# Optimization experiments

Hardware: AMD Instinct MI355X
Metric: run time of the kernel (lower is better)

Reference implementation:

```python
import jax, jax.numpy as jnp
import numpy as np

N_NODES = 50000
N_EDGES = 400000
NFEAT, NHID, NOUT, NCLASS = 512, 256, 256, 8


def _glorot(key, shape):
    lim = float(np.sqrt(6.0 / (shape[0] + shape[1])))
    return jax.random.uniform(key, shape, jnp.float32, -lim, lim)


def setup_inputs() -> dict:
    key = jax.random.key(0)
    ks = jax.random.split(key, 8)
    x = jax.random.normal(ks[0], (N_NODES, NFEAT), jnp.float32)
    edge_index = jax.random.randint(ks[1], (2, N_EDGES), 0, N_NODES, jnp.int32)
    # learnable edge weight logits (init 1 - eps in the module; trained => generic values)
    edge_w_params = jnp.ones((N_EDGES,), jnp.float32) * 0.9999
    W1 = _glorot(ks[2], (NFEAT, NHID)); b1 = jnp.zeros((NHID,), jnp.float32)
    W2 = _glorot(ks[3], (NHID, NHID)); b2 = jnp.zeros((NHID,), jnp.float32)
    W3 = _glorot(ks[4], (NHID, NOUT)); b3 = jnp.zeros((NOUT,), jnp.float32)
    Wlin = _glorot(ks[5], (NHID + NHID + NOUT, NCLASS))
    blin = jnp.zeros((NCLASS,), jnp.float32)
    return {"x": x, "edge_index": edge_index, "edge_w_params": edge_w_params,
            "W1": W1, "b1": b1, "W2": W2, "b2": b2, "W3": W3, "b3": b3,
            "Wlin": Wlin, "blin": blin}


def _gcn_conv(x, W, b, src, dst, ew, n):
    """PyG GCNConv with add_self_loops=True.
    Self-loop weight is 1 (fill_value). norm = d^-1/2[src] * w * d^-1/2[dst].
    Self-loop contribution handled analytically (no edge concat).
    """
    deg = jax.ops.segment_sum(ew, dst, num_segments=n) + 1.0  # +1 self-loop weight
    dinv = jnp.where(deg > 0, jax.lax.rsqrt(deg), 0.0)
    norm = dinv[src] * ew * dinv[dst]                          # [E]
    h = x @ W                                                  # [n, out]
    agg = jax.ops.segment_sum(h[src] * norm[:, None], dst, num_segments=n)
    agg = agg + h * (dinv * dinv)[:, None]                     # self loops
    return agg + b


def reference(x, edge_index, edge_w_params, W1, b1, W2, b2, W3, b3, Wlin, blin):
    n = x.shape[0]
    src, dst = edge_index[0], edge_index[1]
    ew = jax.nn.sigmoid(edge_w_params)
    ones_ew = jnp.ones_like(ew)
    x1 = jax.nn.relu(_gcn_conv(x, W1, b1, src, dst, ew, n))    # dropout: eval mode (identity)
    x2 = jax.nn.relu(_gcn_conv(x1, W2, b2, src, dst, ew, n))
    x3 = _gcn_conv(x2, W3, b3, src, dst, ones_ew, n)           # gc3 called without edge_weight
    logits = jnp.concatenate((x1, x2, x3), axis=1) @ Wlin + blin
    return jax.nn.log_softmax(logits, axis=1)
```

## Files before the change

### kernel.cpp

```cpp
#include <hip/hip_runtime.h>
#include <math.h>

#define N_NODES 50000
#define N_EDGES 400000
#define M_PAD 50048
#define NFEAT 512
#define NHID 256
#define NCLASS 8
#define SCAN_BLOCKS ((N_NODES + 255) / 256)

typedef unsigned short u16;
typedef __attribute__((ext_vector_type(8))) unsigned short u16x8;
typedef __attribute__((ext_vector_type(8))) short s16x8;
typedef __attribute__((ext_vector_type(4))) float f32x4;

__device__ __forceinline__ float bf2f(u16 u) {
    union { unsigned int i; float f; } v; v.i = ((unsigned int)u) << 16; return v.f;
}
__device__ __forceinline__ float bf2f_hi(unsigned int packed) {
    union { unsigned int i; float f; } v; v.i = packed & 0xffff0000u; return v.f;
}
__device__ __forceinline__ float bf2f_lo(unsigned int packed) {
    union { unsigned int i; float f; } v; v.i = packed << 16; return v.f;
}
__device__ __forceinline__ u16 f2bf(float f) {
    union { float f; unsigned int i; } v; v.f = f;
    unsigned int r = v.i + 0x7fffu + ((v.i >> 16) & 1u);
    return (u16)(r >> 16);
}


__global__ void init_k(float* deg, int* cnt, int* cur) {
    int i = blockIdx.x * blockDim.x + threadIdx.x;
    if (i < N_NODES) { deg[i] = 1.0f; cnt[i] = 0; cur[i] = 0; }
}

__global__ void edge_deg_k(const float* __restrict__ p, const int* __restrict__ dst,
                           float* __restrict__ deg, int* __restrict__ cnt,
                           float* __restrict__ ew_out) {
    int e = blockIdx.x * blockDim.x + threadIdx.x;
    if (e >= N_EDGES) return;
    float ew = 1.0f / (1.0f + expf(-p[e]));
    ew_out[e] = ew;
    int d = dst[e];
    atomicAdd(&deg[d], ew);
    atomicAdd(&cnt[d], 1);
}

__global__ void finalize_dinv_k(float* __restrict__ deg, const int* __restrict__ cnt,
                                float* __restrict__ dinv3) {
    int i = blockIdx.x * blockDim.x + threadIdx.x;
    if (i < N_NODES) {
        deg[i]   = 1.0f / sqrtf(deg[i]);
        dinv3[i] = 1.0f / sqrtf(1.0f + (float)cnt[i]);
    }
}

__global__ __launch_bounds__(256) void scan1_k(const int* __restrict__ cnt,
                                               int* __restrict__ row_start,
                                               int* __restrict__ bsum) {
    __shared__ int tmp[256];
    int t = threadIdx.x;
    int g = blockIdx.x * 256 + t;
    int v = (g < N_NODES) ? cnt[g] : 0;
    tmp[t] = v;
    __syncthreads();
    #pragma unroll
    for (int off = 1; off < 256; off <<= 1) {
        int u = (t >= off) ? tmp[t - off] : 0;
        __syncthreads();
        tmp[t] += u;
        __syncthreads();
    }
    if (g < N_NODES) row_start[g] = tmp[t] - v;
    if (t == 255) bsum[blockIdx.x] = tmp[255];
}

__global__ __launch_bounds__(256) void scan2_k(int* __restrict__ bsum) {
    __shared__ int tmp[256];
    int t = threadIdx.x;
    int v = (t < SCAN_BLOCKS) ? bsum[t] : 0;
    tmp[t] = v;
    __syncthreads();
    #pragma unroll
    for (int off = 1; off < 256; off <<= 1) {
        int u = (t >= off) ? tmp[t - off] : 0;
        __syncthreads();
        tmp[t] += u;
        __syncthreads();
    }
    if (t < SCAN_BLOCKS) bsum[t] = tmp[t] - v;
}

__global__ __launch_bounds__(256) void scan3_k(int* __restrict__ row_start,
                                               const int* __restrict__ bsum) {
    int t = threadIdx.x;
    int g = blockIdx.x * 256 + t;
    if (g < N_NODES) row_start[g] += bsum[blockIdx.x];
    if (g == 0) row_start[N_NODES] = N_EDGES;
}

__global__ void fill_k(const int* __restrict__ src, const int* __restrict__ dst,
                       const float* __restrict__ ew, const float* __restrict__ dinv,
                       const float* __restrict__ dinv3,
                       const int* __restrict__ row_start, int* __restrict__ cur,
                       uint2* __restrict__ ep, uint2* __restrict__ ep3) {
    int e = blockIdx.x * blockDim.x + threadIdx.x;
    if (e >= N_EDGES) return;
    int s = src[e], d = dst[e];
    float w  = dinv[s] * ew[e] * dinv[d];
    float w3 = dinv3[s] * dinv3[d];
    int p = atomicAdd(&cur[d], 1);
    int slot = row_start[d] + p;
    ep[slot]  = make_uint2((unsigned int)s, __float_as_uint(w));
    ep3[slot] = make_uint2((unsigned int)s, __float_as_uint(w3));
}


__global__ void wtrans_all_k(const float* __restrict__ W1, const float* __restrict__ W2,
                             const float* __restrict__ W3, u16* __restrict__ wt1,
                             u16* __restrict__ wt2, u16* __restrict__ wt3) {
    int idx = blockIdx.x * 256 + threadIdx.x;
    const float* W; u16* Wt; int K;
    if (idx < 256 * 512)           { W = W1; Wt = wt1; K = 512; }
    else if (idx < 256 * 512 + 256 * 256) { idx -= 256 * 512; W = W2; Wt = wt2; K = 256; }
    else if (idx < 256 * 512 + 2 * 256 * 256) { idx -= 256 * 512 + 256 * 256; W = W3; Wt = wt3; K = 256; }
    else return;
    int n = idx / K, k = idx - n * K;
    Wt[(size_t)n * K + k] = f2bf(W[(size_t)k * 256 + n]);
}

__global__ void zeropad_k(u16* a, u16* b) {
    int i = blockIdx.x * 256 + threadIdx.x;
    if (i < (M_PAD - N_NODES) * 256) {
        a[(size_t)N_NODES * 256 + i] = 0;
        b[(size_t)N_NODES * 256 + i] = 0;
    }
}


__device__ __forceinline__ u16x8 ldcvt_f32(const float* p, bool ok) {
    u16x8 o = {0, 0, 0, 0, 0, 0, 0, 0};
    if (ok) {
        float4 a = *(const float4*)p;
        float4 b = *(const float4*)(p + 4);
        o[0] = f2bf(a.x); o[1] = f2bf(a.y); o[2] = f2bf(a.z); o[3] = f2bf(a.w);
        o[4] = f2bf(b.x); o[5] = f2bf(b.y); o[6] = f2bf(b.z); o[7] = f2bf(b.w);
    }
    return o;
}

template <bool AF32>
__global__ __launch_bounds__(256) void gemm_bf16_k(const void* __restrict__ Ap,
                                                   const u16* __restrict__ BT,
                                                   u16* __restrict__ C, int K) {
    __shared__ u16 Asl[128 * 40];
    __shared__ u16 Bsl[128 * 40];
    int tid = threadIdx.x;
    int lane = tid & 63;
    int wid = tid >> 6;
    int wm = wid >> 1, wn = wid & 1;
    int row0 = blockIdx.x * 128;
    int col0 = blockIdx.y * 128;

    int c0 = tid, c1 = tid + 256;
    int ar0 = c0 >> 2, ak0 = (c0 & 3) << 3;
    int ar1 = c1 >> 2, ak1 = (c1 & 3) << 3;
    const u16*   A16 = (const u16*)Ap;
    const float* A32 = (const float*)Ap;
    bool ok0 = (row0 + ar0) < N_NODES;
    bool ok1 = (row0 + ar1) < N_NODES;
    const u16* Ag0 = A16 + (size_t)(row0 + ar0) * K + ak0;
    const u16* Ag1 = A16 + (size_t)(row0 + ar1) * K + ak1;
    const float* Af0 = A32 + (size_t)(row0 + ar0) * K + ak0;
    const float* Af1 = A32 + (size_t)(row0 + ar1) * K + ak1;
    const u16* Bg0 = BT + (size_t)(col0 + ar0) * K + ak0;
    const u16* Bg1 = BT + (size_t)(col0 + ar1) * K + ak1;
    int la0 = ar0 * 40 + ak0, la1 = ar1 * 40 + ak1;

    u16x8 ra0, ra1;
    if (AF32) { ra0 = ldcvt_f32(Af0, ok0); ra1 = ldcvt_f32(Af1, ok1); }
    else      { ra0 = *(const u16x8*)Ag0;  ra1 = *(const u16x8*)Ag1; }
    u16x8 rb0 = *(const u16x8*)Bg0;
    u16x8 rb1 = *(const u16x8*)Bg1;

    f32x4 acc[4][4] = {};

    int arow = wm * 64 + (lane & 15);
    int bcol = wn * 64 + (lane & 15);
    int kg = (lane >> 4) << 3;

    int nt = K >> 5;
    for (int t = 0; t < nt; ++t) {
        __syncthreads();
        *(u16x8*)&Asl[la0] = ra0; *(u16x8*)&Asl[la1] = ra1;
        *(u16x8*)&Bsl[la0] = rb0; *(u16x8*)&Bsl[la1] = rb1;
        __syncthreads();
        if (t + 1 < nt) {
            int ko = (t + 1) << 5;
            if (AF32) { ra0 = ldcvt_f32(Af0 + ko, ok0); ra1 = ldcvt_f32(Af1 + ko, ok1); }
            else      { ra0 = *(const u16x8*)(Ag0 + ko); ra1 = *(const u16x8*)(Ag1 + ko); }
            rb0 = *(const u16x8*)(Bg0 + ko);
            rb1 = *(const u16x8*)(Bg1 + ko);
        }
        s16x8 af[4], bf[4];
        #pragma unroll
        for (int m = 0; m < 4; ++m)
            af[m] = *(const s16x8*)&Asl[(arow + m * 16) * 40 + kg];
        #pragma unroll
        for (int n = 0; n < 4; ++n)
            bf[n] = *(const s16x8*)&Bsl[(bcol + n * 16) * 40 + kg];
        #pragma unroll
        for (int m = 0; m < 4; ++m)
            #pragma unroll
            for (int n = 0; n < 4; ++n)
                acc[m][n] = __builtin_amdgcn_mfma_f32_16x16x32_bf16(af[m], bf[n], acc[m][n], 0, 0, 0);
    }

    int crow0 = row0 + wm * 64 + ((lane >> 4) << 2);
    int ccol  = col0 + wn * 64 + (lane & 15);
    #pragma unroll
    for (int m = 0; m < 4; ++m)
        #pragma unroll
        for (int n = 0; n < 4; ++n)
            #pragma unroll
            for (int r = 0; r < 4; ++r)
                C[(size_t)(crow0 + m * 16 + r) * 256 + ccol + n * 16] = f2bf(acc[m][n][r]);
}


template <bool RELU>
__global__ __launch_bounds__(256) void gather_k(const u16* __restrict__ h,
                                                const int* __restrict__ row_start,
                                                const uint2* __restrict__ ep,
                                                const float* __restrict__ dinv,
                                                const float* __restrict__ bias,
                                                u16* __restrict__ outb) {
    int node = blockIdx.x * 4 + (threadIdx.x >> 6);
    if (node >= N_NODES) return;
    int lane = threadIdx.x & 63;

    float di = dinv[node];
    float sw = di * di;
    uint2 hv = *(const uint2*)(h + (size_t)node * 256 + lane * 4);
    float4 acc;
    acc.x = bf2f_lo(hv.x) * sw; acc.y = bf2f_hi(hv.x) * sw;
    acc.z = bf2f_lo(hv.y) * sw; acc.w = bf2f_hi(hv.y) * sw;

    int beg = row_start[node], end = row_start[node + 1];
    int j = beg;
    for (; j + 4 <= end; j += 4) {
        uint2 e0 = ep[j], e1 = ep[j + 1], e2 = ep[j + 2], e3 = ep[j + 3];
        uint2 u0 = *(const uint2*)(h + (size_t)e0.x * 256 + lane * 4);
        uint2 u1 = *(const uint2*)(h + (size_t)e1.x * 256 + lane * 4);
        uint2 u2 = *(const uint2*)(h + (size_t)e2.x * 256 + lane * 4);
        uint2 u3 = *(const uint2*)(h + (size_t)e3.x * 256 + lane * 4);
        float w0 = __uint_as_float(e0.y), w1 = __uint_as_float(e1.y);
        float w2 = __uint_as_float(e2.y), w3 = __uint_as_float(e3.y);
        acc.x += bf2f_lo(u0.x) * w0; acc.y += bf2f_hi(u0.x) * w0;
        acc.z += bf2f_lo(u0.y) * w0; acc.w += bf2f_hi(u0.y) * w0;
        acc.x += bf2f_lo(u1.x) * w1; acc.y += bf2f_hi(u1.x) * w1;
        acc.z += bf2f_lo(u1.y) * w1; acc.w += bf2f_hi(u1.y) * w1;
        acc.x += bf2f_lo(u2.x) * w2; acc.y += bf2f_hi(u2.x) * w2;
        acc.z += bf2f_lo(u2.y) * w2; acc.w += bf2f_hi(u2.y) * w2;
        acc.x += bf2f_lo(u3.x) * w3; acc.y += bf2f_hi(u3.x) * w3;
        acc.z += bf2f_lo(u3.y) * w3; acc.w += bf2f_hi(u3.y) * w3;
    }
    for (; j < end; ++j) {
        uint2 e = ep[j];
        float w = __uint_as_float(e.y);
        uint2 uv = *(const uint2*)(h + (size_t)e.x * 256 + lane * 4);
        acc.x += bf2f_lo(uv.x) * w; acc.y += bf2f_hi(uv.x) * w;
        acc.z += bf2f_lo(uv.y) * w; acc.w += bf2f_hi(uv.y) * w;
    }
    float4 bv = ((const float4*)bias)[lane];
    acc.x += bv.x; acc.y += bv.y; acc.z += bv.z; acc.w += bv.w;
    if (RELU) {
        acc.x = fmaxf(acc.x, 0.f); acc.y = fmaxf(acc.y, 0.f);
        acc.z = fmaxf(acc.z, 0.f); acc.w = fmaxf(acc.w, 0.f);
    }
    uint2 o;
    o.x = (unsigned int)f2bf(acc.x) | ((unsigned int)f2bf(acc.y) << 16);
    o.y = (unsigned int)f2bf(acc.z) | ((unsigned int)f2bf(acc.w) << 16);
    *(uint2*)(outb + (size_t)node * 256 + lane * 4) = o;
}


template <bool FIRST>
__global__ __launch_bounds__(256) void logits_acc_k(const u16* __restrict__ x,
                                                    const float* __restrict__ Wlin,
                                                    const float* __restrict__ blin,
                                                    float* __restrict__ logits, int seg) {
    __shared__ float Ws[256 * 8];
    int tid = threadIdx.x;
    const float* Wseg = Wlin + (size_t)seg * 256 * 8;
    for (int i = tid; i < 2048; i += 256) Ws[i] = Wseg[i];
    __syncthreads();
    int row = blockIdx.x * 32 + (tid >> 3);
    int c = tid & 7;
    if (row >= N_NODES) return;
    const u16* xr = x + (size_t)row * 256;
    float acc = 0.f;
    for (int k8 = 0; k8 < 32; ++k8) {
        u16x8 v = *(const u16x8*)&xr[k8 * 8];
        #pragma unroll
        for (int i = 0; i < 8; ++i) acc += bf2f(v[i]) * Ws[(k8 * 8 + i) * 8 + c];
    }
    float* lp = &logits[(size_t)row * 8 + c];
    if (FIRST) *lp = acc + blin[c];
    else       *lp += acc;
}

__global__ void log_softmax_k(const float* __restrict__ logits, float* __restrict__ out) {
    int row = blockIdx.x * blockDim.x + threadIdx.x;
    if (row >= N_NODES) return;
    float4 a = *(const float4*)&logits[(size_t)row * 8];
    float4 b = *(const float4*)&logits[(size_t)row * 8 + 4];
    float m = fmaxf(fmaxf(fmaxf(a.x, a.y), fmaxf(a.z, a.w)),
                    fmaxf(fmaxf(b.x, b.y), fmaxf(b.z, b.w)));
    float s = expf(a.x - m) + expf(a.y - m) + expf(a.z - m) + expf(a.w - m)
            + expf(b.x - m) + expf(b.y - m) + expf(b.z - m) + expf(b.w - m);
    float ls = logf(s) + m;
    float* o = &out[(size_t)row * 8];
    o[0] = a.x - ls; o[1] = a.y - ls; o[2] = a.z - ls; o[3] = a.w - ls;
    o[4] = b.x - ls; o[5] = b.y - ls; o[6] = b.z - ls; o[7] = b.w - ls;
}


extern "C" void kernel_launch(void* const* d_in, const int* in_sizes, int n_in,
                              void* d_out, int out_size, void* d_ws, size_t ws_size,
                              hipStream_t stream) {
    const float* x    = (const float*)d_in[0];
    const int*   ei   = (const int*)d_in[1];
    const float* ewp  = (const float*)d_in[2];
    const float* W1   = (const float*)d_in[3];
    const float* b1   = (const float*)d_in[4];
    const float* W2   = (const float*)d_in[5];
    const float* b2   = (const float*)d_in[6];
    const float* W3   = (const float*)d_in[7];
    const float* b3   = (const float*)d_in[8];
    const float* Wlin = (const float*)d_in[9];
    const float* blin = (const float*)d_in[10];
    float* out = (float*)d_out;

    const int* src = ei;
    const int* dst = ei + N_EDGES;

    float* ws = (float*)d_ws;
    float* ew     = ws;
    float* dinv   = ew + N_EDGES;
    float* dinv3  = dinv + N_NODES;
    float* logits = dinv3 + N_NODES;
    int* cnt       = (int*)(logits + (size_t)N_NODES * 8);
    int* cur       = cnt + N_NODES;
    int* row_start = cur + N_NODES;
    int* bsum      = row_start + N_NODES + 1;
    uint2* ep  = (uint2*)(((uintptr_t)(bsum + SCAN_BLOCKS) + 127) & ~(uintptr_t)127);
    uint2* ep3 = ep + N_EDGES;
    u16* hb  = (u16*)(ep3 + N_EDGES);
    u16* x1b = hb  + (size_t)M_PAD * 256;
    u16* x2b = x1b + (size_t)M_PAD * 256;
    u16* x3b = x2b + (size_t)M_PAD * 256;
    u16* wt1 = x3b + (size_t)M_PAD * 256;
    u16* wt2 = wt1 + 256 * 512;
    u16* wt3 = wt2 + 256 * 256;

    dim3 blk(256);
    int nodeBlocks  = (N_NODES + 255) / 256;
    int edgeBlocks  = (N_EDGES + 255) / 256;
    int gathBlocks  = (N_NODES + 3) / 4;
    int rowBlocks32 = (N_NODES + 31) / 32;
    dim3 gemmGrid(M_PAD / 128, 2);

    init_k<<<nodeBlocks, blk, 0, stream>>>(dinv, cnt, cur);
    edge_deg_k<<<edgeBlocks, blk, 0, stream>>>(ewp, dst, dinv, cnt, ew);
    finalize_dinv_k<<<nodeBlocks, blk, 0, stream>>>(dinv, cnt, dinv3);
    scan1_k<<<SCAN_BLOCKS, blk, 0, stream>>>(cnt, row_start, bsum);
    scan2_k<<<1, blk, 0, stream>>>(bsum);
    scan3_k<<<SCAN_BLOCKS, blk, 0, stream>>>(row_start, bsum);
    fill_k<<<edgeBlocks, blk, 0, stream>>>(src, dst, ew, dinv, dinv3, row_start, cur, ep, ep3);

    wtrans_all_k<<<(256 * 512 + 2 * 256 * 256 + 255) / 256, blk, 0, stream>>>(
        W1, W2, W3, wt1, wt2, wt3);
    zeropad_k<<<48, blk, 0, stream>>>(x1b, x2b);

    gemm_bf16_k<true><<<gemmGrid, blk, 0, stream>>>(x, wt1, hb, NFEAT);
    gather_k<true><<<gathBlocks, blk, 0, stream>>>(hb, row_start, ep, dinv, b1, x1b);
    logits_acc_k<true><<<rowBlocks32, blk, 0, stream>>>(x1b, Wlin, blin, logits, 0);

    gemm_bf16_k<false><<<gemmGrid, blk, 0, stream>>>(x1b, wt2, hb, NHID);
    gather_k<true><<<gathBlocks, blk, 0, stream>>>(hb, row_start, ep, dinv, b2, x2b);
    logits_acc_k<false><<<rowBlocks32, blk, 0, stream>>>(x2b, Wlin, blin, logits, 1);

    gemm_bf16_k<false><<<gemmGrid, blk, 0, stream>>>(x2b, wt3, hb, NHID);
    gather_k<false><<<gathBlocks, blk, 0, stream>>>(hb, row_start, ep3, dinv3, b3, x3b);
    logits_acc_k<false><<<rowBlocks32, blk, 0, stream>>>(x3b, Wlin, blin, logits, 2);

    log_softmax_k<<<nodeBlocks, blk, 0, stream>>>(logits, out);
}
```

Baseline: 319.1 us.

## Fold scan fixup into consumers, merge setup kernels, fuse softmax, unroll gather

Drops the scan3 pass. Fill and gather now add the per-block offset bsum[node>>8] to row_start as they read it, and scan2 writes the final row_start sentinel. The weight-transpose and zero-pad kernels are merged into one launch, and log-softmax is folded into the last logits kernel using shuffles across the 8 class lanes. The gather loop is unrolled to 8 edges to keep more loads in flight. Together these remove three launches and some global traffic, at the cost of an extra bsum lookup on every CSR access and higher register pressure in gather.

```diff
diff --git a/kernel.cpp b/kernel.cpp
--- a/kernel.cpp
+++ b/kernel.cpp
@@ -76,7 +76,8 @@
     if (t == 255) bsum[blockIdx.x] = tmp[255];
 }
 
-__global__ __launch_bounds__(256) void scan2_k(int* __restrict__ bsum) {
+__global__ __launch_bounds__(256) void scan2_k(int* __restrict__ bsum,
+                                               int* __restrict__ row_start) {
     __shared__ int tmp[256];
     int t = threadIdx.x;
     int v = (t < SCAN_BLOCKS) ? bsum[t] : 0;
@@ -90,20 +91,14 @@
         __syncthreads();
     }
     if (t < SCAN_BLOCKS) bsum[t] = tmp[t] - v;
-}
-
-__global__ __launch_bounds__(256) void scan3_k(int* __restrict__ row_start,
-                                               const int* __restrict__ bsum) {
-    int t = threadIdx.x;
-    int g = blockIdx.x * 256 + t;
-    if (g < N_NODES) row_start[g] += bsum[blockIdx.x];
-    if (g == 0) row_start[N_NODES] = N_EDGES;
+    if (t == SCAN_BLOCKS - 1) row_start[N_NODES] = v;
 }
 
 __global__ void fill_k(const int* __restrict__ src, const int* __restrict__ dst,
                        const float* __restrict__ ew, const float* __restrict__ dinv,
                        const float* __restrict__ dinv3,
-                       const int* __restrict__ row_start, int* __restrict__ cur,
+                       const int* __restrict__ row_start, const int* __restrict__ bsum,
+                       int* __restrict__ cur,
                        uint2* __restrict__ ep, uint2* __restrict__ ep3) {
     int e = blockIdx.x * blockDim.x + threadIdx.x;
     if (e >= N_EDGES) return;
@@ -111,30 +106,33 @@
     float w  = dinv[s] * ew[e] * dinv[d];
     float w3 = dinv3[s] * dinv3[d];
     int p = atomicAdd(&cur[d], 1);
-    int slot = row_start[d] + p;
+    int slot = row_start[d] + bsum[d >> 8] + p;
     ep[slot]  = make_uint2((unsigned int)s, __float_as_uint(w));
     ep3[slot] = make_uint2((unsigned int)s, __float_as_uint(w3));
 }
 
 
-__global__ void wtrans_all_k(const float* __restrict__ W1, const float* __restrict__ W2,
-                             const float* __restrict__ W3, u16* __restrict__ wt1,
-                             u16* __restrict__ wt2, u16* __restrict__ wt3) {
+#define WT_TOTAL (256 * 512 + 2 * 256 * 256)
+#define ZP_TOTAL ((M_PAD - N_NODES) * 256)
+
+__global__ void wtrans_zp_k(const float* __restrict__ W1, const float* __restrict__ W2,
+                            const float* __restrict__ W3, u16* __restrict__ wt1,
+                            u16* __restrict__ wt2, u16* __restrict__ wt3,
+                            u16* __restrict__ zp_a, u16* __restrict__ zp_b) {
     int idx = blockIdx.x * 256 + threadIdx.x;
-    const float* W; u16* Wt; int K;
-    if (idx < 256 * 512)           { W = W1; Wt = wt1; K = 512; }
-    else if (idx < 256 * 512 + 256 * 256) { idx -= 256 * 512; W = W2; Wt = wt2; K = 256; }
-    else if (idx < 256 * 512 + 2 * 256 * 256) { idx -= 256 * 512 + 256 * 256; W = W3; Wt = wt3; K = 256; }
-    else return;
-    int n = idx / K, k = idx - n * K;
-    Wt[(size_t)n * K + k] = f2bf(W[(size_t)k * 256 + n]);
-}
-
-__global__ void zeropad_k(u16* a, u16* b) {
-    int i = blockIdx.x * 256 + threadIdx.x;
-    if (i < (M_PAD - N_NODES) * 256) {
-        a[(size_t)N_NODES * 256 + i] = 0;
-        b[(size_t)N_NODES * 256 + i] = 0;
+    if (idx < WT_TOTAL) {
+        const float* W; u16* Wt; int K;
+        if (idx < 256 * 512)                  { W = W1; Wt = wt1; K = 512; }
+        else if (idx < 256 * 512 + 256 * 256) { idx -= 256 * 512; W = W2; Wt = wt2; K = 256; }
+        else                                  { idx -= 256 * 512 + 256 * 256; W = W3; Wt = wt3; K = 256; }
+        int n = idx / K, k = idx - n * K;
+        Wt[(size_t)n * K + k] = f2bf(W[(size_t)k * 256 + n]);
+        return;
+    }
+    int z = idx - WT_TOTAL;
+    if (z < ZP_TOTAL) {
+        zp_a[(size_t)N_NODES * 256 + z] = 0;
+        zp_b[(size_t)N_NODES * 256 + z] = 0;
     }
 }
 
@@ -178,14 +176,13 @@
     const u16* Bg1 = BT + (size_t)(col0 + ar1) * K + ak1;
     int la0 = ar0 * 40 + ak0, la1 = ar1 * 40 + ak1;
 
-    u16x8 ra0, ra1;
+    u16x8 ra0, ra1, rb0, rb1;
     if (AF32) { ra0 = ldcvt_f32(Af0, ok0); ra1 = ldcvt_f32(Af1, ok1); }
     else      { ra0 = *(const u16x8*)Ag0;  ra1 = *(const u16x8*)Ag1; }
-    u16x8 rb0 = *(const u16x8*)Bg0;
-    u16x8 rb1 = *(const u16x8*)Bg1;
+    rb0 = *(const u16x8*)Bg0;
+    rb1 = *(const u16x8*)Bg1;
 
     f32x4 acc[4][4] = {};
-
     int arow = wm * 64 + (lane & 15);
     int bcol = wn * 64 + (lane & 15);
     int kg = (lane >> 4) << 3;
@@ -229,9 +226,15 @@
 }
 
 
+__device__ __forceinline__ void fma4(float4& acc, uint2 u, float w) {
+    acc.x += bf2f_lo(u.x) * w; acc.y += bf2f_hi(u.x) * w;
+    acc.z += bf2f_lo(u.y) * w; acc.w += bf2f_hi(u.y) * w;
+}
+
 template <bool RELU>
 __global__ __launch_bounds__(256) void gather_k(const u16* __restrict__ h,
                                                 const int* __restrict__ row_start,
+                                                const int* __restrict__ bsum,
                                                 const uint2* __restrict__ ep,
                                                 const float* __restrict__ dinv,
                                                 const float* __restrict__ bias,
@@ -247,31 +250,38 @@
     acc.x = bf2f_lo(hv.x) * sw; acc.y = bf2f_hi(hv.x) * sw;
     acc.z = bf2f_lo(hv.y) * sw; acc.w = bf2f_hi(hv.y) * sw;
 
-    int beg = row_start[node], end = row_start[node + 1];
+    int beg = row_start[node] + bsum[node >> 8];
+    int end = row_start[node + 1] + bsum[(node + 1) >> 8];
     int j = beg;
+    for (; j + 8 <= end; j += 8) {
+        uint2 e0 = ep[j],     e1 = ep[j + 1], e2 = ep[j + 2], e3 = ep[j + 3];
+        uint2 e4 = ep[j + 4], e5 = ep[j + 5], e6 = ep[j + 6], e7 = ep[j + 7];
+        uint2 u0 = *(const uint2*)(h + (size_t)e0.x * 256 + lane * 4);
+        uint2 u1 = *(const uint2*)(h + (size_t)e1.x * 256 + lane * 4);
+        uint2 u2 = *(const uint2*)(h + (size_t)e2.x * 256 + lane * 4);
+        uint2 u3 = *(const uint2*)(h + (size_t)e3.x * 256 + lane * 4);
+        uint2 u4 = *(const uint2*)(h + (size_t)e4.x * 256 + lane * 4);
+        uint2 u5 = *(const uint2*)(h + (size_t)e5.x * 256 + lane * 4);
+        uint2 u6 = *(const uint2*)(h + (size_t)e6.x * 256 + lane * 4);
+        uint2 u7 = *(const uint2*)(h + (size_t)e7.x * 256 + lane * 4);
+        fma4(acc, u0, __uint_as_float(e0.y)); fma4(acc, u1, __uint_as_float(e1.y));
+        fma4(acc, u2, __uint_as_float(e2.y)); fma4(acc, u3, __uint_as_float(e3.y));
+        fma4(acc, u4, __uint_as_float(e4.y)); fma4(acc, u5, __uint_as_float(e5.y));
+        fma4(acc, u6, __uint_as_float(e6.y)); fma4(acc, u7, __uint_as_float(e7.y));
+    }
     for (; j + 4 <= end; j += 4) {
         uint2 e0 = ep[j], e1 = ep[j + 1], e2 = ep[j + 2], e3 = ep[j + 3];
         uint2 u0 = *(const uint2*)(h + (size_t)e0.x * 256 + lane * 4);
         uint2 u1 = *(const uint2*)(h + (size_t)e1.x * 256 + lane * 4);
         uint2 u2 = *(const uint2*)(h + (size_t)e2.x * 256 + lane * 4);
         uint2 u3 = *(const uint2*)(h + (size_t)e3.x * 256 + lane * 4);
-        float w0 = __uint_as_float(e0.y), w1 = __uint_as_float(e1.y);
-        float w2 = __uint_as_float(e2.y), w3 = __uint_as_float(e3.y);
-        acc.x += bf2f_lo(u0.x) * w0; acc.y += bf2f_hi(u0.x) * w0;
-        acc.z += bf2f_lo(u0.y) * w0; acc.w += bf2f_hi(u0.y) * w0;
-        acc.x += bf2f_lo(u1.x) * w1; acc.y += bf2f_hi(u1.x) * w1;
-        acc.z += bf2f_lo(u1.y) * w1; acc.w += bf2f_hi(u1.y) * w1;
-        acc.x += bf2f_lo(u2.x) * w2; acc.y += bf2f_hi(u2.x) * w2;
-        acc.z += bf2f_lo(u2.y) * w2; acc.w += bf2f_hi(u2.y) * w2;
-        acc.x += bf2f_lo(u3.x) * w3; acc.y += bf2f_hi(u3.x) * w3;
-        acc.z += bf2f_lo(u3.y) * w3; acc.w += bf2f_hi(u3.y) * w3;
+        fma4(acc, u0, __uint_as_float(e0.y)); fma4(acc, u1, __uint_as_float(e1.y));
+        fma4(acc, u2, __uint_as_float(e2.y)); fma4(acc, u3, __uint_as_float(e3.y));
     }
     for (; j < end; ++j) {
         uint2 e = ep[j];
-        float w = __uint_as_float(e.y);
-        uint2 uv = *(const uint2*)(h + (size_t)e.x * 256 + lane * 4);
-        acc.x += bf2f_lo(uv.x) * w; acc.y += bf2f_hi(uv.x) * w;
-        acc.z += bf2f_lo(uv.y) * w; acc.w += bf2f_hi(uv.y) * w;
+        uint2 u = *(const uint2*)(h + (size_t)e.x * 256 + lane * 4);
+        fma4(acc, u, __uint_as_float(e.y));
     }
     float4 bv = ((const float4*)bias)[lane];
     acc.x += bv.x; acc.y += bv.y; acc.z += bv.z; acc.w += bv.w;
@@ -286,11 +296,12 @@
 }
 
 
-template <bool FIRST>
+template <int MODE>
 __global__ __launch_bounds__(256) void logits_acc_k(const u16* __restrict__ x,
                                                     const float* __restrict__ Wlin,
                                                     const float* __restrict__ blin,
-                                                    float* __restrict__ logits, int seg) {
+                                                    float* __restrict__ logits,
+                                                    float* __restrict__ out, int seg) {
     __shared__ float Ws[256 * 8];
     int tid = threadIdx.x;
     const float* Wseg = Wlin + (size_t)seg * 256 * 8;
@@ -307,23 +318,22 @@
         for (int i = 0; i < 8; ++i) acc += bf2f(v[i]) * Ws[(k8 * 8 + i) * 8 + c];
     }
     float* lp = &logits[(size_t)row * 8 + c];
-    if (FIRST) *lp = acc + blin[c];
-    else       *lp += acc;
-}
-
-__global__ void log_softmax_k(const float* __restrict__ logits, float* __restrict__ out) {
-    int row = blockIdx.x * blockDim.x + threadIdx.x;
-    if (row >= N_NODES) return;
-    float4 a = *(const float4*)&logits[(size_t)row * 8];
-    float4 b = *(const float4*)&logits[(size_t)row * 8 + 4];
-    float m = fmaxf(fmaxf(fmaxf(a.x, a.y), fmaxf(a.z, a.w)),
-                    fmaxf(fmaxf(b.x, b.y), fmaxf(b.z, b.w)));
-    float s = expf(a.x - m) + expf(a.y - m) + expf(a.z - m) + expf(a.w - m)
-            + expf(b.x - m) + expf(b.y - m) + expf(b.z - m) + expf(b.w - m);
-    float ls = logf(s) + m;
-    float* o = &out[(size_t)row * 8];
-    o[0] = a.x - ls; o[1] = a.y - ls; o[2] = a.z - ls; o[3] = a.w - ls;
-    o[4] = b.x - ls; o[5] = b.y - ls; o[6] = b.z - ls; o[7] = b.w - ls;
+    if (MODE == 0) {
+        *lp = acc + blin[c];
+    } else if (MODE == 1) {
+        *lp += acc;
+    } else {
+        float t = *lp + acc;
+        float m = t;
+        m = fmaxf(m, __shfl_xor(m, 1));
+        m = fmaxf(m, __shfl_xor(m, 2));
+        m = fmaxf(m, __shfl_xor(m, 4));
+        float s = expf(t - m);
+        s += __shfl_xor(s, 1);
+        s += __shfl_xor(s, 2);
+        s += __shfl_xor(s, 4);
+        out[(size_t)row * 8 + c] = t - (logf(s) + m);
+    }
 }
 
 
@@ -376,25 +386,22 @@
     edge_deg_k<<<edgeBlocks, blk, 0, stream>>>(ewp, dst, dinv, cnt, ew);
     finalize_dinv_k<<<nodeBlocks, blk, 0, stream>>>(dinv, cnt, dinv3);
     scan1_k<<<SCAN_BLOCKS, blk, 0, stream>>>(cnt, row_start, bsum);
-    scan2_k<<<1, blk, 0, stream>>>(bsum);
-    scan3_k<<<SCAN_BLOCKS, blk, 0, stream>>>(row_start, bsum);
-    fill_k<<<edgeBlocks, blk, 0, stream>>>(src, dst, ew, dinv, dinv3, row_start, cur, ep, ep3);
-
-    wtrans_all_k<<<(256 * 512 + 2 * 256 * 256 + 255) / 256, blk, 0, stream>>>(
-        W1, W2, W3, wt1, wt2, wt3);
-    zeropad_k<<<48, blk, 0, stream>>>(x1b, x2b);
+    scan2_k<<<1, blk, 0, stream>>>(bsum, row_start);
+    fill_k<<<edgeBlocks, blk, 0, stream>>>(src, dst, ew, dinv, dinv3, row_start, bsum,
+                                           cur, ep, ep3);
+
+    wtrans_zp_k<<<(WT_TOTAL + ZP_TOTAL + 255) / 256, blk, 0, stream>>>(
+        W1, W2, W3, wt1, wt2, wt3, x1b, x2b);
 
     gemm_bf16_k<true><<<gemmGrid, blk, 0, stream>>>(x, wt1, hb, NFEAT);
-    gather_k<true><<<gathBlocks, blk, 0, stream>>>(hb, row_start, ep, dinv, b1, x1b);
-    logits_acc_k<true><<<rowBlocks32, blk, 0, stream>>>(x1b, Wlin, blin, logits, 0);
+    gather_k<true><<<gathBlocks, blk, 0, stream>>>(hb, row_start, bsum, ep, dinv, b1, x1b);
+    logits_acc_k<0><<<rowBlocks32, blk, 0, stream>>>(x1b, Wlin, blin, logits, nullptr, 0);
 
     gemm_bf16_k<false><<<gemmGrid, blk, 0, stream>>>(x1b, wt2, hb, NHID);
-    gather_k<true><<<gathBlocks, blk, 0, stream>>>(hb, row_start, ep, dinv, b2, x2b);
-    logits_acc_k<false><<<rowBlocks32, blk, 0, stream>>>(x2b, Wlin, blin, logits, 1);
+    gather_k<true><<<gathBlocks, blk, 0, stream>>>(hb, row_start, bsum, ep, dinv, b2, x2b);
+    logits_acc_k<1><<<rowBlocks32, blk, 0, stream>>>(x2b, Wlin, blin, logits, nullptr, 1);
 
     gemm_bf16_k<false><<<gemmGrid, blk, 0, stream>>>(x2b, wt3, hb, NHID);
-    gather_k<false><<<gathBlocks, blk, 0, stream>>>(hb, row_start, ep3, dinv3, b3, x3b);
-    logits_acc_k<false><<<rowBlocks32, blk, 0, stream>>>(x3b, Wlin, blin, logits, 2);
-
-    log_softmax_k<<<nodeBlocks, blk, 0, stream>>>(logits, out);
-}
+    gather_k<false><<<gathBlocks, blk, 0, stream>>>(hb, row_start, bsum, ep3, dinv3, b3, x3b);
+    logits_acc_k<2><<<rowBlocks32, blk, 0, stream>>>(x3b, Wlin, blin, logits, out, 2);
+}
```

Result: faster. 311.8 us (-2.3%).
